# Performance work log

Hardware: AMD Instinct MI355X
Metric: run time of the kernel (lower is better)

## Reference

```python
import jax, jax.numpy as jnp
import numpy as np

GRID_RES = 64
BOUND = 1.2

def _coords():
    lin = jnp.linspace(-BOUND, BOUND, GRID_RES, dtype=jnp.float32)
    gx, gy, gz = jnp.meshgrid(lin, lin, lin, indexing='ij')
    return jnp.stack([gx, gy, gz], axis=-1).reshape(-1, 3)  # (R^3, 3)

def setup_inputs() -> dict:
    key = jax.random.key(0)
    ks = jax.random.split(key, 9)
    B, D, H = 2, 512, 512
    s_in = 1.0 / np.sqrt(D + 3)
    s_h = 1.0 / np.sqrt(H)
    return {
        'cad_latent': jax.random.normal(ks[0], (B, D), jnp.float32),
        'W0': jax.random.normal(ks[1], (D + 3, H), jnp.float32) * s_in,
        'b0': jax.random.normal(ks[2], (H,), jnp.float32) * s_in,
        'W1': jax.random.normal(ks[3], (H, H), jnp.float32) * s_h,
        'b1': jax.random.normal(ks[4], (H,), jnp.float32) * s_h,
        'W2': jax.random.normal(ks[5], (H, H), jnp.float32) * s_h,
        'b2': jax.random.normal(ks[6], (H,), jnp.float32) * s_h,
        'W3': jax.random.normal(ks[7], (H, 1), jnp.float32) * s_h,
        'b3': jax.random.normal(ks[8], (1,), jnp.float32) * s_h,
    }

def reference(cad_latent, W0, b0, W1, b1, W2, b2, W3, b3):
    B, D = cad_latent.shape
    coords = _coords()  # (P, 3), P = R^3
    # First layer: concat([latent, coords]) @ W0 decomposed to avoid
    # materializing the broadcast-concatenated (B, P, D+3) tensor.
    lat_part = cad_latent @ W0[:D]          # (B, H)
    coord_part = coords @ W0[D:]            # (P, H)
    h = jax.nn.silu(lat_part[:, None, :] + coord_part[None, :, :] + b0)  # (B, P, H)
    h = jax.nn.silu(h @ W1 + b1)
    h = jax.nn.silu(h @ W2 + b2)
    sdf = h @ W3 + b3                       # (B, P, 1)
    return sdf.reshape(B, GRID_RES, GRID_RES, GRID_RES)
```

## Files before the change

### kernel.cpp

```cpp
#include <hip/hip_runtime.h>

#define H 512
#define MTILE 32
#define NBLK 16384
#define STEPC (2.4f / 63.0f)

typedef _Float16 half8 __attribute__((ext_vector_type(8)));
typedef _Float16 half4_t __attribute__((ext_vector_type(4)));
typedef float floatx16 __attribute__((ext_vector_type(16)));
typedef float floatx4 __attribute__((ext_vector_type(4)));
typedef float floatx2 __attribute__((ext_vector_type(2)));

__device__ inline float silu_f(float x) {
    return __fdividef(x, 1.0f + __expf(-x));
}

__global__ void prep_latw(const float* __restrict__ lat, const float* __restrict__ W0,
                          const float* __restrict__ b0, float* __restrict__ latw) {
    __shared__ float sl[H];
    const int b = blockIdx.x;
    const int j = threadIdx.x;
    sl[j] = lat[b * H + j];
    __syncthreads();
    float acc = b0[j];
#pragma unroll 8
    for (int d = 0; d < H; ++d) acc += sl[d] * W0[d * H + j];
    latw[b * H + j] = acc;
}

__global__ void prep_w16(const float* __restrict__ W1, const float* __restrict__ W2,
                         _Float16* __restrict__ ws) {
    const int id = blockIdx.x * 512 + threadIdx.x;
    const int l = id >> 18;
    const int rem = id & 0x3FFFF;
    const int k = rem >> 9, n = rem & 511;
    const float w = (l == 0 ? W1 : W2)[rem];
    ws[((size_t)(l * 64 + (k >> 3)) * 512 + n) * 8 + (k & 7)] = (_Float16)w;
}

__global__ __launch_bounds__(256, 4) void mesh_main(
    const float* __restrict__ W0, const float* __restrict__ b1,
    const float* __restrict__ b2, const float* __restrict__ W3,
    const float* __restrict__ b3, const float* __restrict__ latw,
    const _Float16* __restrict__ wsB, float* __restrict__ out) {

    __shared__ _Float16 hbuf2[2048 * 8];
    __shared__ float lwbuf[2 * H];
    __shared__ float partials[4][MTILE];

    const int tid = threadIdx.x;
    const int wave = tid >> 6, lane = tid & 63;
    const int lm = lane & 31, hi = lane >> 5;
    const int bi = blockIdx.x;
    const int b = bi >> 13;
    const int p0 = (bi & 8191) << 5;
    const float c0 = -1.2f + (float)(p0 >> 12) * STEPC;
    const float c1 = -1.2f + (float)((p0 >> 6) & 63) * STEPC;
    const float z0 = -1.2f + (float)(p0 & 63) * STEPC;

#pragma unroll
    for (int it = 0; it < 2; ++it) {
        const int j = tid + it * 256;
        const float lwv = latw[b * H + j]
                        + c0 * W0[(H + 0) * H + j]
                        + c1 * W0[(H + 1) * H + j];
        floatx2 v;
        v[0] = lwv;
        v[1] = W0[(H + 2) * H + j];
        *(floatx2*)&lwbuf[2 * j] = v;
    }
    __syncthreads();

    {
        const float c2v = z0 + (float)lm * STEPC;
#pragma unroll
        for (int s = 0; s < 8; ++s) {
            const int g = wave * 16 + hi * 8 + s;
            const floatx4* lp = (const floatx4*)&lwbuf[g * 16];
            half8 hv;
#pragma unroll
            for (int i = 0; i < 4; ++i) {
                const floatx4 pv = lp[i];
                hv[2 * i + 0] = (_Float16)silu_f(pv[0] + c2v * pv[1]);
                hv[2 * i + 1] = (_Float16)silu_f(pv[2] + c2v * pv[3]);
            }
            *(half8*)&hbuf2[(g * 32 + lm) * 8] = hv;
        }
    }

    const _Float16* hb = hbuf2 + hi * 256 + lm * 8;
    const _Float16* wsl = wsB + ((size_t)hi * 512 + wave * 128 + lm) * 8;

    floatx16 acc[4];

    auto zero_acc = [&]() {
#pragma unroll
        for (int j = 0; j < 4; ++j)
#pragma unroll
            for (int r = 0; r < 16; ++r) acc[j][r] = 0.f;
    };

    auto loadW = [&](int l, int ks, half8 (&wf)[4]) {
        const _Float16* p = wsl + (size_t)(l * 32 + ks) * 8192;
#pragma unroll
        for (int j = 0; j < 4; ++j)
            wf[j] = *(const half8*)(p + j * 256);
    };

    auto compute = [&](half8 (&wf)[4], half8 a) {
#pragma unroll
        for (int j = 0; j < 4; ++j)
            acc[j] = __builtin_amdgcn_mfma_f32_32x32x16_f16(wf[j], a, acc[j], 0, 0, 0);
    };

    auto run_gemm = [&](int l) {
        half8 Wb0[4], Wb1[4], a0, a1;
        loadW(l, 0, Wb0); a0 = *(const half8*)(hb + 0 * 512);
        loadW(l, 1, Wb1); a1 = *(const half8*)(hb + 1 * 512);
#pragma unroll 1
        for (int ks = 0; ks < 30; ks += 2) {
            compute(Wb0, a0);
            loadW(l, ks + 2, Wb0); a0 = *(const half8*)(hb + (ks + 2) * 512);
            compute(Wb1, a1);
            loadW(l, ks + 3, Wb1); a1 = *(const half8*)(hb + (ks + 3) * 512);
        }
        compute(Wb0, a0);
        compute(Wb1, a1);
    };

    zero_acc();
    __syncthreads();
    run_gemm(0);
    __syncthreads();
    {
        _Float16* wb = hbuf2 + lm * 8 + hi * 4;
#pragma unroll
        for (int j = 0; j < 4; ++j)
#pragma unroll
            for (int g = 0; g < 4; ++g) {
                const floatx4 b1v = *(const floatx4*)&b1[wave * 128 + j * 32 + g * 8 + hi * 4];
                half4_t hv;
#pragma unroll
                for (int r = 0; r < 4; ++r)
                    hv[r] = (_Float16)silu_f(acc[j][g * 4 + r] + b1v[r]);
                *(half4_t*)(wb + (wave * 16 + j * 4 + g) * 256) = hv;
            }
    }

    zero_acc();
    __syncthreads();
    run_gemm(1);

    {
        float sum = 0.f;
#pragma unroll
        for (int j = 0; j < 4; ++j)
#pragma unroll
            for (int g = 0; g < 4; ++g) {
                const int n0 = wave * 128 + j * 32 + g * 8 + hi * 4;
                const floatx4 b2v = *(const floatx4*)&b2[n0];
                const floatx4 w3v = *(const floatx4*)&W3[n0];
#pragma unroll
                for (int r = 0; r < 4; ++r)
                    sum += silu_f(acc[j][g * 4 + r] + b2v[r]) * w3v[r];
            }
        sum += __shfl_xor(sum, 32);
        if (hi == 0) partials[wave][lm] = sum;
    }
    __syncthreads();
    if (tid < MTILE) {
        float o = b3[0];
#pragma unroll
        for (int w = 0; w < 4; ++w) o += partials[w][tid];
        out[(size_t)bi * MTILE + tid] = o;
    }
}

extern "C" void kernel_launch(void* const* d_in, const int* in_sizes, int n_in,
                              void* d_out, int out_size, void* d_ws, size_t ws_size,
                              hipStream_t stream) {
    const float* lat = (const float*)d_in[0];
    const float* W0  = (const float*)d_in[1];
    const float* b0  = (const float*)d_in[2];
    const float* W1  = (const float*)d_in[3];
    const float* b1  = (const float*)d_in[4];
    const float* W2  = (const float*)d_in[5];
    const float* b2  = (const float*)d_in[6];
    const float* W3  = (const float*)d_in[7];
    const float* b3  = (const float*)d_in[8];
    float* out = (float*)d_out;

    float* latw = (float*)d_ws;
    _Float16* wsB = (_Float16*)((char*)d_ws + 4096);

    prep_latw<<<2, 512, 0, stream>>>(lat, W0, b0, latw);
    prep_w16<<<1024, 512, 0, stream>>>(W1, W2, wsB);
    mesh_main<<<NBLK, 256, 0, stream>>>(W0, b1, b2, W3, b3, latw, wsB, out);
}
```

Before: 909.6 us.

## Split N across 8 waves per block and fuse the two prep kernels

Each block now runs 512 threads (8 waves), and each wave computes 64 output columns instead of 128. This halves the accumulator registers so more waves can be resident (launch bounds 512,6). The weight layout is reorganized so each wave's slice is contiguous per k-step. The latent-projection and fp16 weight-conversion prep kernels are merged into one launch to save a kernel launch. The trade-off is that each wave now does half as many MFMAs per A-fragment load from LDS, so LDS traffic per FLOP rises. The output index mapping was also reworked.

```diff
diff --git a/kernel.cpp b/kernel.cpp
--- a/kernel.cpp
+++ b/kernel.cpp
@@ -15,30 +15,34 @@
     return __fdividef(x, 1.0f + __expf(-x));
 }
 
-__global__ void prep_latw(const float* __restrict__ lat, const float* __restrict__ W0,
-                          const float* __restrict__ b0, float* __restrict__ latw) {
+__global__ void prep_fused(const float* __restrict__ lat, const float* __restrict__ W0,
+                           const float* __restrict__ b0,
+                           const float* __restrict__ W1, const float* __restrict__ W2,
+                           float* __restrict__ latw, _Float16* __restrict__ ws) {
     __shared__ float sl[H];
-    const int b = blockIdx.x;
-    const int j = threadIdx.x;
-    sl[j] = lat[b * H + j];
-    __syncthreads();
-    float acc = b0[j];
+    if (blockIdx.x < 1024) {
+        const int id = blockIdx.x * 512 + threadIdx.x;
+        const int l = id >> 18;
+        const int rem = id & 0x3FFFF;
+        const int k = rem >> 9, n = rem & 511;
+        const float w = (l == 0 ? W1 : W2)[rem];
+        const int ks = k >> 4, hi = (k >> 3) & 1, e = k & 7;
+        const int wv = n >> 6, nt = (n >> 5) & 1, lm = n & 31;
+        ws[(size_t)(l * 8 + wv) * 32768 + hi * 16384 + ks * 512 + nt * 256 + lm * 8 + e]
+            = (_Float16)w;
+    } else {
+        const int b = blockIdx.x - 1024;
+        const int j = threadIdx.x;
+        sl[j] = lat[b * H + j];
+        __syncthreads();
+        float acc = b0[j];
 #pragma unroll 8
-    for (int d = 0; d < H; ++d) acc += sl[d] * W0[d * H + j];
-    latw[b * H + j] = acc;
-}
-
-__global__ void prep_w16(const float* __restrict__ W1, const float* __restrict__ W2,
-                         _Float16* __restrict__ ws) {
-    const int id = blockIdx.x * 512 + threadIdx.x;
-    const int l = id >> 18;
-    const int rem = id & 0x3FFFF;
-    const int k = rem >> 9, n = rem & 511;
-    const float w = (l == 0 ? W1 : W2)[rem];
-    ws[((size_t)(l * 64 + (k >> 3)) * 512 + n) * 8 + (k & 7)] = (_Float16)w;
-}
-
-__global__ __launch_bounds__(256, 4) void mesh_main(
+        for (int d = 0; d < H; ++d) acc += sl[d] * W0[d * H + j];
+        latw[b * H + j] = acc;
+    }
+}
+
+__global__ __launch_bounds__(512, 6) void mesh_main(
     const float* __restrict__ W0, const float* __restrict__ b1,
     const float* __restrict__ b2, const float* __restrict__ W3,
     const float* __restrict__ b3, const float* __restrict__ latw,
@@ -46,21 +50,22 @@
 
     __shared__ _Float16 hbuf2[2048 * 8];
     __shared__ float lwbuf[2 * H];
-    __shared__ float partials[4][MTILE];
+    __shared__ float partials[8][MTILE];
 
     const int tid = threadIdx.x;
     const int wave = tid >> 6, lane = tid & 63;
     const int lm = lane & 31, hi = lane >> 5;
+    const int uwave = __builtin_amdgcn_readfirstlane(wave);
     const int bi = blockIdx.x;
     const int b = bi >> 13;
-    const int p0 = (bi & 8191) << 5;
-    const float c0 = -1.2f + (float)(p0 >> 12) * STEPC;
-    const float c1 = -1.2f + (float)((p0 >> 6) & 63) * STEPC;
-    const float z0 = -1.2f + (float)(p0 & 63) * STEPC;
-
-#pragma unroll
-    for (int it = 0; it < 2; ++it) {
-        const int j = tid + it * 256;
+    const int xy = (bi >> 1) & 4095;
+    const int zh = bi & 1;
+    const float c0 = -1.2f + (float)(xy >> 6) * STEPC;
+    const float c1 = -1.2f + (float)(xy & 63) * STEPC;
+    const float z0 = -1.2f + (float)(zh << 5) * STEPC;
+
+    {
+        const int j = tid;
         const float lwv = latw[b * H + j]
                         + c0 * W0[(H + 0) * H + j]
                         + c1 * W0[(H + 1) * H + j];
@@ -74,8 +79,8 @@
     {
         const float c2v = z0 + (float)lm * STEPC;
 #pragma unroll
-        for (int s = 0; s < 8; ++s) {
-            const int g = wave * 16 + hi * 8 + s;
+        for (int s = 0; s < 4; ++s) {
+            const int g = (wave * 2 + hi) * 4 + s;
             const floatx4* lp = (const floatx4*)&lwbuf[g * 16];
             half8 hv;
 #pragma unroll
@@ -89,40 +94,43 @@
     }
 
     const _Float16* hb = hbuf2 + hi * 256 + lm * 8;
-    const _Float16* wsl = wsB + ((size_t)hi * 512 + wave * 128 + lm) * 8;
-
-    floatx16 acc[4];
+    const _Float16* wsl0 = wsB + (size_t)uwave * 32768 + hi * 16384 + lm * 8;
+
+    floatx16 acc[2];
 
     auto zero_acc = [&]() {
 #pragma unroll
-        for (int j = 0; j < 4; ++j)
-#pragma unroll
-            for (int r = 0; r < 16; ++r) acc[j][r] = 0.f;
-    };
-
-    auto loadW = [&](int l, int ks, half8 (&wf)[4]) {
-        const _Float16* p = wsl + (size_t)(l * 32 + ks) * 8192;
-#pragma unroll
-        for (int j = 0; j < 4; ++j)
-            wf[j] = *(const half8*)(p + j * 256);
-    };
-
-    auto compute = [&](half8 (&wf)[4], half8 a) {
-#pragma unroll
-        for (int j = 0; j < 4; ++j)
-            acc[j] = __builtin_amdgcn_mfma_f32_32x32x16_f16(wf[j], a, acc[j], 0, 0, 0);
-    };
-
-    auto run_gemm = [&](int l) {
-        half8 Wb0[4], Wb1[4], a0, a1;
-        loadW(l, 0, Wb0); a0 = *(const half8*)(hb + 0 * 512);
-        loadW(l, 1, Wb1); a1 = *(const half8*)(hb + 1 * 512);
+        for (int nt = 0; nt < 2; ++nt)
+#pragma unroll
+            for (int r = 0; r < 16; ++r) acc[nt][r] = 0.f;
+    };
+
+    auto loadW = [&](const _Float16* base, int ks, half8 (&wf)[2]) {
+        const _Float16* p = base + ks * 512;
+        wf[0] = *(const half8*)(p);
+        wf[1] = *(const half8*)(p + 256);
+    };
+
+    auto loadA = [&](int ks) -> half8 {
+        return *(const half8*)(hb + ks * 512);
+    };
+
+    auto compute = [&](half8 (&wf)[2], half8 a) {
+#pragma unroll
+        for (int nt = 0; nt < 2; ++nt)
+            acc[nt] = __builtin_amdgcn_mfma_f32_32x32x16_f16(wf[nt], a, acc[nt], 0, 0, 0);
+    };
+
+    auto run_gemm = [&](const _Float16* base) {
+        half8 Wb0[2], Wb1[2], a0, a1;
+        loadW(base, 0, Wb0); a0 = loadA(0);
+        loadW(base, 1, Wb1); a1 = loadA(1);
 #pragma unroll 1
         for (int ks = 0; ks < 30; ks += 2) {
             compute(Wb0, a0);
-            loadW(l, ks + 2, Wb0); a0 = *(const half8*)(hb + (ks + 2) * 512);
+            loadW(base, ks + 2, Wb0); a0 = loadA(ks + 2);
             compute(Wb1, a1);
-            loadW(l, ks + 3, Wb1); a1 = *(const half8*)(hb + (ks + 3) * 512);
+            loadW(base, ks + 3, Wb1); a1 = loadA(ks + 3);
         }
         compute(Wb0, a0);
         compute(Wb1, a1);
@@ -130,39 +138,38 @@
 
     zero_acc();
     __syncthreads();
-    run_gemm(0);
-    __syncthreads();
-    {
-        _Float16* wb = hbuf2 + lm * 8 + hi * 4;
-#pragma unroll
-        for (int j = 0; j < 4; ++j)
+    run_gemm(wsl0);
+    __syncthreads();
+    {
+        _Float16* wb = hbuf2 + (wave * 8) * 256 + lm * 8 + hi * 4;
+#pragma unroll
+        for (int nt = 0; nt < 2; ++nt)
 #pragma unroll
             for (int g = 0; g < 4; ++g) {
-                const floatx4 b1v = *(const floatx4*)&b1[wave * 128 + j * 32 + g * 8 + hi * 4];
+                const floatx4 b1v = *(const floatx4*)&b1[wave * 64 + nt * 32 + g * 8 + hi * 4];
                 half4_t hv;
 #pragma unroll
-                for (int r = 0; r < 4; ++r)
-                    hv[r] = (_Float16)silu_f(acc[j][g * 4 + r] + b1v[r]);
-                *(half4_t*)(wb + (wave * 16 + j * 4 + g) * 256) = hv;
+                for (int j = 0; j < 4; ++j)
+                    hv[j] = (_Float16)silu_f(acc[nt][g * 4 + j] + b1v[j]);
+                *(half4_t*)(wb + (nt * 4 + g) * 256) = hv;
             }
     }
 
     zero_acc();
     __syncthreads();
-    run_gemm(1);
-
+    run_gemm(wsl0 + 8 * 32768);
     {
         float sum = 0.f;
 #pragma unroll
-        for (int j = 0; j < 4; ++j)
+        for (int nt = 0; nt < 2; ++nt)
 #pragma unroll
             for (int g = 0; g < 4; ++g) {
-                const int n0 = wave * 128 + j * 32 + g * 8 + hi * 4;
+                const int n0 = wave * 64 + nt * 32 + g * 8 + hi * 4;
                 const floatx4 b2v = *(const floatx4*)&b2[n0];
                 const floatx4 w3v = *(const floatx4*)&W3[n0];
 #pragma unroll
-                for (int r = 0; r < 4; ++r)
-                    sum += silu_f(acc[j][g * 4 + r] + b2v[r]) * w3v[r];
+                for (int j = 0; j < 4; ++j)
+                    sum += silu_f(acc[nt][g * 4 + j] + b2v[j]) * w3v[j];
             }
         sum += __shfl_xor(sum, 32);
         if (hi == 0) partials[wave][lm] = sum;
@@ -171,8 +178,8 @@
     if (tid < MTILE) {
         float o = b3[0];
 #pragma unroll
-        for (int w = 0; w < 4; ++w) o += partials[w][tid];
-        out[(size_t)bi * MTILE + tid] = o;
+        for (int w = 0; w < 8; ++w) o += partials[w][tid];
+        out[(size_t)(bi >> 1) * 64 + (bi & 1) * 32 + tid] = o;
     }
 }
 
@@ -193,7 +200,6 @@
     float* latw = (float*)d_ws;
     _Float16* wsB = (_Float16*)((char*)d_ws + 4096);
 
-    prep_latw<<<2, 512, 0, stream>>>(lat, W0, b0, latw);
-    prep_w16<<<1024, 512, 0, stream>>>(W1, W2, wsB);
-    mesh_main<<<NBLK, 256, 0, stream>>>(W0, b1, b2, W3, b3, latw, wsB, out);
-}
+    prep_fused<<<1026, 512, 0, stream>>>(lat, W0, b0, W1, W2, latw, wsB);
+    mesh_main<<<NBLK, 512, 0, stream>>>(W0, b1, b2, W3, b3, latw, wsB, out);
+}
```

Result: no change. 904.4 us (-0.6%).
